# Kernel tuning notes

Measured on AMD Instinct MI355X. Metric: run time of the kernel, lower is better.

## Reference

```python
import jax, jax.numpy as jnp
import numpy as np

N, E, D, H = 50000, 800000, 128, 4
DH = D // H
BN_EPS = 1e-5


def setup_inputs() -> dict:
    key = jax.random.key(0)
    ks = jax.random.split(key, 16)
    s = 0.02
    inp = {
        "x": jax.random.normal(ks[0], (N, D), dtype=jnp.float32),
        "edge_index": jax.random.randint(ks[1], (2, E), 0, N, dtype=jnp.int64),
        "Wk": jax.random.normal(ks[2], (D, D), dtype=jnp.float32) * s,
        "bk": jnp.zeros((D,), jnp.float32),
        "Wm": jax.random.normal(ks[3], (D, D), dtype=jnp.float32) * s,
        "bm": jnp.zeros((D,), jnp.float32),
        "Wq": jax.random.normal(ks[4], (D, D), dtype=jnp.float32) * s,
        "bq": jnp.zeros((D,), jnp.float32),
        "W1": jax.random.normal(ks[5], (D, D), dtype=jnp.float32) * s,
        "b1": jnp.zeros((D,), jnp.float32),
        "gamma": jnp.ones((D,), jnp.float32),
        "beta": jnp.zeros((D,), jnp.float32),
        "W2": jax.random.normal(ks[6], (D, D), dtype=jnp.float32) * s,
        "b2": jnp.zeros((D,), jnp.float32),
    }
    return inp


def reference(x, edge_index, Wk, bk, Wm, bm, Wq, bq, W1, b1, gamma, beta, W2, b2):
    src = edge_index[0]  # [E] softmax segment key
    dst = edge_index[1]  # [E] aggregation target
    x_i = x[dst]         # [E, D] (torch code: X[1])
    x_j = x[src]         # [E, D] (torch code: X[0])

    key = (x_i @ Wk + bk).reshape(-1, H, DH)
    msg = (x_j @ Wm + bm).reshape(-1, H, DH)
    query = (x_j @ Wq + bq).reshape(-1, H, DH) / jnp.sqrt(jnp.float32(DH))

    scores = jnp.sum(query * key, axis=2)  # [E, H]

    # segment softmax over src node index (numerically stable)
    smax = jax.ops.segment_max(scores, src, num_segments=N)
    e = jnp.exp(scores - smax[src])
    ssum = jax.ops.segment_sum(e, src, num_segments=N)
    alpha = e / ssum[src]  # [E, H]

    # rescale by per-src-node edge count
    cnt = jax.ops.segment_sum(jnp.ones((scores.shape[0],), jnp.float32), src, num_segments=N)
    alpha = alpha * cnt[src][:, None]

    out_e = (msg * alpha[:, :, None]).reshape(-1, D)  # [E, D]
    out = jax.ops.segment_sum(out_e, dst, num_segments=N)  # [N, D]

    # MLP: Linear -> BatchNorm1d (training-mode batch stats) -> ReLU -> Linear
    h = out @ W1 + b1
    mean = jnp.mean(h, axis=0)
    var = jnp.var(h, axis=0)  # biased variance, as torch BN uses for normalization
    h = (h - mean) * jax.lax.rsqrt(var + BN_EPS) * gamma + beta
    h = jax.nn.relu(h)
    return h @ W2 + b2
```

## Files before the change

### kernel.cpp

```cpp
#include <hip/hip_runtime.h>
#include <hip/hip_bf16.h>

#define N_NODES 50000
#define N_EDGES 800000
#define DIM 128
#define NHEAD 4
#define GEMM_BLOCKS 782
#define RANK_ILP 8
#define RANK_BLOCKS 391

typedef __bf16 bf16x8 __attribute__((ext_vector_type(8)));
typedef __bf16 bf16x2 __attribute__((ext_vector_type(2)));
typedef float f32x4 __attribute__((ext_vector_type(4)));

struct WPtrs { const float* w[5]; };

__global__ __launch_bounds__(256) void prep_weights(WPtrs P, __bf16* __restrict__ Wt)
{
  __shared__ __bf16 tileT[16][136];
  const int mat = blockIdx.x >> 3, sl = blockIdx.x & 7;
  const float* W = P.w[mat];
  const int col0 = sl * 16;
  const int t = threadIdx.x;
  #pragma unroll
  for (int i = 0; i < 8; ++i) {
    int id = t + i * 256;
    int k = id >> 4, c = id & 15;
    tileT[c][k] = (__bf16)W[k * 128 + col0 + c];
  }
  __syncthreads();
  int c = t >> 4, kb = t & 15;
  bf16x8 v = *(const bf16x8*)&tileT[c][kb * 8];
  *(bf16x8*)&Wt[(size_t)mat * 16384 + (size_t)(col0 + c) * 128 + kb * 8] = v;
}


__device__ __forceinline__ void stage_Wt_half(const __bf16* __restrict__ Wt,
    int half, __bf16 (*wLDS)[136])
{
  const int t = threadIdx.x;
  const __bf16* base = Wt + (size_t)half * 64 * 128;
  #pragma unroll
  for (int i = 0; i < 4; ++i) {
    int id = t + i * 256;
    int col = id >> 4, kb = id & 15;
    bf16x8 v = ((const bf16x8*)(base + (size_t)col * 128))[kb];
    *(bf16x8*)&wLDS[col][kb * 8] = v;
  }
}

__device__ __forceinline__ void stage_A_f32(const float* __restrict__ A, int row0,
    int nrows, __bf16 (*aLDS)[136])
{
  const int t = threadIdx.x;
  #pragma unroll
  for (int i = 0; i < 4; ++i) {
    int id = t + i * 256;
    int r = id >> 4, cb = id & 15;
    int gr = row0 + r;
    float4 v0 = make_float4(0.f, 0.f, 0.f, 0.f), v1 = v0;
    if (gr < nrows) {
      const float4* row = (const float4*)(A + (size_t)gr * DIM);
      v0 = row[cb * 2];
      v1 = row[cb * 2 + 1];
    }
    bf16x8 o;
    o[0] = (__bf16)v0.x; o[1] = (__bf16)v0.y; o[2] = (__bf16)v0.z; o[3] = (__bf16)v0.w;
    o[4] = (__bf16)v1.x; o[5] = (__bf16)v1.y; o[6] = (__bf16)v1.z; o[7] = (__bf16)v1.w;
    *(bf16x8*)&aLDS[r][cb * 8] = o;
  }
}

__device__ __forceinline__ void mfma_half(const __bf16 (*aLDS)[136],
    const __bf16 (*wLDS)[136], int half, f32x4 acc[8])
{
  const int lane = threadIdx.x & 63, wave = threadIdx.x >> 6;
  const int m = lane & 15, q = lane >> 4;
  #pragma unroll
  for (int kt = 0; kt < 4; ++kt) {
    bf16x8 a = *(const bf16x8*)&aLDS[wave * 16 + m][kt * 32 + q * 8];
    #pragma unroll
    for (int ct = 0; ct < 4; ++ct) {
      bf16x8 b = *(const bf16x8*)&wLDS[ct * 16 + m][kt * 32 + q * 8];
      acc[half * 4 + ct] =
          __builtin_amdgcn_mfma_f32_16x16x32_bf16(a, b, acc[half * 4 + ct], 0, 0, 0);
    }
  }
}

template <typename OutT>
__device__ __forceinline__ void store_tile(f32x4 acc[8],
    const float* __restrict__ bias, float scale, OutT* __restrict__ C,
    int row0, int nrows)
{
  const int lane = threadIdx.x & 63, wave = threadIdx.x >> 6;
  const int m = lane & 15, q = lane >> 4;
  #pragma unroll
  for (int j = 0; j < 8; ++j) {
    int col = (j >> 2) * 64 + (j & 3) * 16 + m;
    float bv = bias[col];
    #pragma unroll
    for (int r = 0; r < 4; ++r) {
      int row = row0 + wave * 16 + q * 4 + r;
      if (row < nrows) C[(size_t)row * DIM + col] = (OutT)((acc[j][r] + bv) * scale);
    }
  }
}

__device__ __forceinline__ void gemm_pass(const __bf16 (*aLDS)[136],
    __bf16 (*wLDS)[136], const __bf16* __restrict__ Wt, f32x4 acc[8])
{
  #pragma unroll
  for (int i = 0; i < 8; ++i) acc[i] = (f32x4){0.f, 0.f, 0.f, 0.f};
  stage_Wt_half(Wt, 0, wLDS);
  __syncthreads();
  mfma_half(aLDS, wLDS, 0, acc);
  __syncthreads();
  stage_Wt_half(Wt, 1, wLDS);
  __syncthreads();
  mfma_half(aLDS, wLDS, 1, acc);
}

__global__ __launch_bounds__(256) void qkm_gemm(const float* __restrict__ A,
    const __bf16* __restrict__ Wt,
    const float* __restrict__ bk, const float* __restrict__ bm,
    const float* __restrict__ bq,
    __bf16* __restrict__ Kn, __bf16* __restrict__ Mn, __bf16* __restrict__ Qn)
{
  __shared__ __bf16 aLDS[64][136];
  __shared__ __bf16 wLDS[64][136];
  const int row0 = blockIdx.x * 64;
  f32x4 acc[8];

  stage_A_f32(A, row0, N_NODES, aLDS);
  gemm_pass(aLDS, wLDS, Wt, acc);
  store_tile<__bf16>(acc, bk, 1.0f, Kn, row0, N_NODES);
  __syncthreads();
  gemm_pass(aLDS, wLDS, Wt + 16384, acc);
  store_tile<__bf16>(acc, bm, 1.0f, Mn, row0, N_NODES);
  __syncthreads();
  gemm_pass(aLDS, wLDS, Wt + 32768, acc);
  store_tile<__bf16>(acc, bq, 0.17677669529663689f, Qn, row0, N_NODES);
}

__global__ __launch_bounds__(256) void edge_rank(const int* __restrict__ ei,
    int* __restrict__ deg, int2* __restrict__ rank)
{
  const int base = blockIdx.x * (256 * RANK_ILP) + threadIdx.x;
  int s[RANK_ILP], d[RANK_ILP], rS[RANK_ILP], rD[RANK_ILP];
  #pragma unroll
  for (int i = 0; i < RANK_ILP; ++i) {
    int e = base + i * 256;
    if (e < N_EDGES) { s[i] = ei[e]; d[i] = ei[N_EDGES + e]; }
  }
  #pragma unroll
  for (int i = 0; i < RANK_ILP; ++i) {
    int e = base + i * 256;
    if (e < N_EDGES) rS[i] = atomicAdd(&deg[s[i]], 1);
  }
  #pragma unroll
  for (int i = 0; i < RANK_ILP; ++i) {
    int e = base + i * 256;
    if (e < N_EDGES) rD[i] = atomicAdd(&deg[N_NODES + d[i]], 1);
  }
  #pragma unroll
  for (int i = 0; i < RANK_ILP; ++i) {
    int e = base + i * 256;
    if (e < N_EDGES) rank[e] = make_int2(rS[i], rD[i]);
  }
}

__global__ __launch_bounds__(256) void scan_pass1(const int* __restrict__ deg,
    int* __restrict__ bsum, int total)
{
  int i = blockIdx.x * 256 + threadIdx.x;
  int v = (i < total) ? deg[i] : 0;
  __shared__ int s[256];
  s[threadIdx.x] = v; __syncthreads();
  for (int o = 128; o > 0; o >>= 1) {
    if (threadIdx.x < o) s[threadIdx.x] += s[threadIdx.x + o];
    __syncthreads();
  }
  if (threadIdx.x == 0) bsum[blockIdx.x] = s[0];
}

__global__ __launch_bounds__(512) void scan_pass2(int* __restrict__ bsum, int nblocks)
{
  int t = threadIdx.x;
  __shared__ int s[512];
  int v = (t < nblocks) ? bsum[t] : 0;
  s[t] = v; __syncthreads();
  for (int o = 1; o < 512; o <<= 1) {
    int x = (t >= o) ? s[t - o] : 0;
    __syncthreads();
    s[t] += x;
    __syncthreads();
  }
  bsum[t] = s[t] - v;
}

__global__ __launch_bounds__(256) void scan_pass3(const int* __restrict__ deg,
    const int* __restrict__ bsum, int* __restrict__ starts, int total)
{
  int t = threadIdx.x, i = blockIdx.x * 256 + t;
  int v = (i < total) ? deg[i] : 0;
  __shared__ int s[256];
  s[t] = v; __syncthreads();
  for (int o = 1; o < 256; o <<= 1) {
    int x = (t >= o) ? s[t - o] : 0;
    __syncthreads();
    s[t] += x;
    __syncthreads();
  }
  if (i < total) starts[i] = bsum[blockIdx.x] + s[t] - v;
}

__global__ __launch_bounds__(256) void edge_place(const int* __restrict__ ei,
    const int2* __restrict__ rank, const int* __restrict__ starts,
    int* __restrict__ elistS, int2* __restrict__ elistD)
{
  int e = blockIdx.x * 256 + threadIdx.x;
  int src = ei[e], dst = ei[N_EDGES + e];
  int2 r = rank[e];
  int pS = starts[src] + r.x;
  int pD = starts[N_NODES + dst] - N_EDGES + r.y;
  elistS[pS] = dst;
  elistD[pD] = make_int2(src, pS);
}

__global__ __launch_bounds__(256) void src_scores(const int* __restrict__ starts,
    const int* __restrict__ degS, const int* __restrict__ elistS,
    const __bf16* __restrict__ Qn, const __bf16* __restrict__ Kn,
    __bf16* __restrict__ Mn, float* __restrict__ wexp)
{
  const int wave = threadIdx.x >> 6, l = threadIdx.x & 63;
  const int n = blockIdx.x * 4 + wave;
  const int g = l >> 4, il = l & 15;
  const int h = il >> 2;
  const int beg = starts[n], end = beg + degS[n];
  if (beg == end) return;

  bf16x8 q8 = ((const bf16x8*)(Qn + (size_t)n * DIM))[il];
  float wsum = 0.f;

  for (int p0 = beg; p0 < end; p0 += 16) {
    int pp[4], dd[4];
    #pragma unroll
    for (int u = 0; u < 4; ++u) {
      pp[u] = p0 + u * 4 + g;
      dd[u] = elistS[min(pp[u], end - 1)];
    }
    bf16x8 kk[4];
    #pragma unroll
    for (int u = 0; u < 4; ++u)
      kk[u] = ((const bf16x8*)(Kn + (size_t)dd[u] * DIM))[il];
    #pragma unroll
    for (int u = 0; u < 4; ++u) {
      float pr = 0.f;
      #pragma unroll
      for (int j = 0; j < 8; ++j) pr += (float)q8[j] * (float)kk[u][j];
      pr += __shfl_xor(pr, 1);
      pr += __shfl_xor(pr, 2);
      float w = (pp[u] < end) ? __expf(pr) : 0.f;
      wsum += w;
      if ((pp[u] < end) && (il & 3) == 0) wexp[(size_t)pp[u] * NHEAD + h] = w;
    }
  }
  wsum += __shfl_xor(wsum, 16);
  wsum += __shfl_xor(wsum, 32);
  float factor = (float)(end - beg) / wsum;

  float fm = __shfl(factor, (l >> 4) << 2);
  bf16x2* mrow = (bf16x2*)(Mn + (size_t)n * DIM);
  bf16x2 mv = mrow[l];
  mv[0] = (__bf16)((float)mv[0] * fm);
  mv[1] = (__bf16)((float)mv[1] * fm);
  mrow[l] = mv;
}

__global__ __launch_bounds__(256) void dst_aggregate(const int* __restrict__ startsD,
    const int* __restrict__ degD, const int2* __restrict__ elistD,
    const __bf16* __restrict__ Mn, const float* __restrict__ wexp,
    float* __restrict__ agg)
{
  const int wave = threadIdx.x >> 6, l = threadIdx.x & 63;
  const int n = blockIdx.x * 4 + wave;
  const int g = l >> 4, il = l & 15;
  const int h = il >> 2;
  const int beg = startsD[n] - N_EDGES, end = beg + degD[n];

  float acc[8];
  #pragma unroll
  for (int j = 0; j < 8; ++j) acc[j] = 0.f;

  for (int q0 = beg; q0 < end; q0 += 16) {
    int qq[4]; int2 ss[4];
    #pragma unroll
    for (int u = 0; u < 4; ++u) {
      qq[u] = q0 + u * 4 + g;
      ss[u] = elistD[min(qq[u], end - 1)];
    }
    float aa[4];
    #pragma unroll
    for (int u = 0; u < 4; ++u) aa[u] = wexp[(size_t)ss[u].y * NHEAD + h];
    bf16x8 mm[4];
    #pragma unroll
    for (int u = 0; u < 4; ++u)
      mm[u] = ((const bf16x8*)(Mn + (size_t)ss[u].x * DIM))[il];
    #pragma unroll
    for (int u = 0; u < 4; ++u) {
      float av = (qq[u] < end) ? aa[u] : 0.f;
      #pragma unroll
      for (int j = 0; j < 8; ++j) acc[j] += (float)mm[u][j] * av;
    }
  }
  #pragma unroll
  for (int j = 0; j < 8; ++j) {
    acc[j] += __shfl_xor(acc[j], 16);
    acc[j] += __shfl_xor(acc[j], 32);
  }
  if (g == 0) {
    float* row = agg + (size_t)n * DIM + il * 8;
    *(float4*)row       = make_float4(acc[0], acc[1], acc[2], acc[3]);
    *(float4*)(row + 4) = make_float4(acc[4], acc[5], acc[6], acc[7]);
  }
}

__global__ __launch_bounds__(256) void gemm_stats(const float* __restrict__ A,
    const __bf16* __restrict__ Wt, const float* __restrict__ bias,
    __bf16* __restrict__ C, float* __restrict__ colsum, float* __restrict__ colsq)
{
  __shared__ __bf16 aLDS[64][136];
  __shared__ __bf16 wLDS[64][136];
  __shared__ float csum[128], csq[128];
  const int t = threadIdx.x;
  const int row0 = blockIdx.x * 64;

  stage_A_f32(A, row0, N_NODES, aLDS);
  if (t < 128) { csum[t] = 0.f; csq[t] = 0.f; }
  f32x4 acc[8];
  gemm_pass(aLDS, wLDS, Wt, acc);

  const int lane = t & 63, wave = t >> 6;
  const int m = lane & 15, q = lane >> 4;
  #pragma unroll
  for (int j = 0; j < 8; ++j) {
    int col = (j >> 2) * 64 + (j & 3) * 16 + m;
    float bv = bias[col];
    float s = 0.f, s2 = 0.f;
    #pragma unroll
    for (int r = 0; r < 4; ++r) {
      int row = row0 + wave * 16 + q * 4 + r;
      float hv = acc[j][r] + bv;
      if (row < N_NODES) {
        C[(size_t)row * DIM + col] = (__bf16)hv;
        s += hv; s2 += hv * hv;
      }
    }
    s  += __shfl_xor(s, 16);  s  += __shfl_xor(s, 32);
    s2 += __shfl_xor(s2, 16); s2 += __shfl_xor(s2, 32);
    if (q == 0) {
      atomicAdd(&csum[col], s);
      atomicAdd(&csq[col], s2);
    }
  }
  __syncthreads();
  if (t < 128) {
    atomicAdd(&colsum[t], csum[t]);
    atomicAdd(&colsq[t], csq[t]);
  }
}

__global__ __launch_bounds__(256) void gemm_bn(const __bf16* __restrict__ A,
    const __bf16* __restrict__ Wt, const float* __restrict__ bias,
    float* __restrict__ C, const float* __restrict__ colsum,
    const float* __restrict__ colsq, const float* __restrict__ gamma,
    const float* __restrict__ beta)
{
  __shared__ __bf16 aLDS[64][136];
  __shared__ __bf16 wLDS[64][136];
  __shared__ float sA[128], sB[128];
  const int t = threadIdx.x;
  const int row0 = blockIdx.x * 64;

  if (t < 128) {
    float mean = colsum[t] * (1.0f / N_NODES);
    float var = colsq[t] * (1.0f / N_NODES) - mean * mean;
    float inv = rsqrtf(var + 1e-5f);
    float a = gamma[t] * inv;
    sA[t] = a;
    sB[t] = beta[t] - mean * a;
  }
  __syncthreads();

  {
    const int cb = t & 15;
    float sa[8], sb[8];
    #pragma unroll
    for (int j = 0; j < 8; ++j) { sa[j] = sA[cb * 8 + j]; sb[j] = sB[cb * 8 + j]; }
    #pragma unroll
    for (int i = 0; i < 4; ++i) {
      int id = t + i * 256;
      int r = id >> 4;
      int gr = row0 + r;
      bf16x8 v = {};
      if (gr < N_NODES) v = ((const bf16x8*)(A + (size_t)gr * DIM))[cb];
      bf16x8 o;
      #pragma unroll
      for (int j = 0; j < 8; ++j)
        o[j] = (__bf16)fmaxf((float)v[j] * sa[j] + sb[j], 0.f);
      *(bf16x8*)&aLDS[r][cb * 8] = o;
    }
  }
  f32x4 acc[8];
  gemm_pass(aLDS, wLDS, Wt, acc);
  store_tile<float>(acc, bias, 1.0f, C, row0, N_NODES);
}

extern "C" void kernel_launch(void* const* d_in, const int* in_sizes, int n_in,
                              void* d_out, int out_size, void* d_ws, size_t ws_size,
                              hipStream_t stream) {
  const float* x     = (const float*)d_in[0];
  const int*   ei    = (const int*)d_in[1];
  const float* Wk    = (const float*)d_in[2];
  const float* bk    = (const float*)d_in[3];
  const float* Wm    = (const float*)d_in[4];
  const float* bm    = (const float*)d_in[5];
  const float* Wq    = (const float*)d_in[6];
  const float* bq    = (const float*)d_in[7];
  const float* W1    = (const float*)d_in[8];
  const float* b1    = (const float*)d_in[9];
  const float* gamma = (const float*)d_in[10];
  const float* beta  = (const float*)d_in[11];
  const float* W2    = (const float*)d_in[12];
  const float* b2    = (const float*)d_in[13];

  float* ws = (float*)d_ws;
  const size_t ND  = (size_t)N_NODES * DIM;
  const size_t NDh = ND / 2;
  const size_t EH  = (size_t)N_EDGES * NHEAD;
  const int    N2  = 2 * N_NODES;

  __bf16* Kn   = (__bf16*)ws;
  __bf16* Mn   = (__bf16*)(ws + NDh);
  __bf16* Qn   = (__bf16*)(ws + 2 * NDh);
  float*  agg  = ws + 3 * NDh;
  __bf16* h1   = (__bf16*)(agg + ND);
  float*  wexp = (float*)(h1 + ND);
  int2*   rank   = (int2*)(wexp + EH);
  int2*   elistD = rank + N_EDGES;
  int*    elistS = (int*)(elistD + N_EDGES);
  int*    deg    = elistS + N_EDGES;
  float*  colsum = (float*)(deg + N2);
  float*  colsq  = colsum + 128;
  int*    starts = (int*)(colsq + 128);
  int*    bsum   = starts + N2;
  __bf16* Wt     = (__bf16*)(bsum + 512);
  float*  outp   = (float*)d_out;

  hipMemsetAsync(deg, 0, (N2 + 256) * sizeof(int), stream);

  const int scan_blocks = (N2 + 255) / 256;
  const int edge_blocks = N_EDGES / 256;
  const int node_blocks = N_NODES / 4;

  WPtrs wp; wp.w[0] = Wk; wp.w[1] = Wm; wp.w[2] = Wq; wp.w[3] = W1; wp.w[4] = W2;
  prep_weights<<<40, 256, 0, stream>>>(wp, Wt);

  edge_rank<<<RANK_BLOCKS, 256, 0, stream>>>(ei, deg, rank);
  scan_pass1<<<scan_blocks, 256, 0, stream>>>(deg, bsum, N2);
  scan_pass2<<<1, 512, 0, stream>>>(bsum, scan_blocks);
  scan_pass3<<<scan_blocks, 256, 0, stream>>>(deg, bsum, starts, N2);
  edge_place<<<edge_blocks, 256, 0, stream>>>(ei, rank, starts, elistS, elistD);

  qkm_gemm<<<GEMM_BLOCKS, 256, 0, stream>>>(x, Wt, bk, bm, bq, Kn, Mn, Qn);

  src_scores<<<node_blocks, 256, 0, stream>>>(starts, deg, elistS, Qn, Kn, Mn, wexp);
  dst_aggregate<<<node_blocks, 256, 0, stream>>>(starts + N_NODES, deg + N_NODES,
                                                 elistD, Mn, wexp, agg);

  gemm_stats<<<GEMM_BLOCKS, 256, 0, stream>>>(agg, Wt + 3 * 16384, b1, h1,
                                              colsum, colsq);
  gemm_bn<<<GEMM_BLOCKS, 256, 0, stream>>>(h1, Wt + 4 * 16384, b2, outp,
                                           colsum, colsq, gamma, beta);
}
```

Baseline: 350.1 us.

## Merge edge ranking with QKM GEMM in one launch and store aggregate as bf16

Puts the atomic edge-ranking blocks and the Q/K/M projection GEMM blocks into a single heterogeneous kernel, so the latency-bound atomic work and the compute-bound GEMM can run on the GPU at the same time instead of one after the other. Separately, the aggregated node features are now stored as bf16 instead of fp32, which halves the write in dst_aggregate and the read in gemm_stats (that GEMM already rounds its input to bf16). The cost is extra rounding of the aggregate before it is staged, which matches the rounding that was already applied in LDS, and a larger grid whose GEMM blocks use more LDS than the ranking blocks need.

```diff
diff --git a/kernel.cpp b/kernel.cpp
--- a/kernel.cpp
+++ b/kernel.cpp
@@ -71,6 +71,21 @@
   }
 }
 
+__device__ __forceinline__ void stage_A_bf16(const __bf16* __restrict__ A, int row0,
+    int nrows, __bf16 (*aLDS)[136])
+{
+  const int t = threadIdx.x;
+  #pragma unroll
+  for (int i = 0; i < 4; ++i) {
+    int id = t + i * 256;
+    int r = id >> 4, cb = id & 15;
+    int gr = row0 + r;
+    bf16x8 v = {};
+    if (gr < nrows) v = ((const bf16x8*)(A + (size_t)gr * DIM))[cb];
+    *(bf16x8*)&aLDS[r][cb * 8] = v;
+  }
+}
+
 __device__ __forceinline__ void mfma_half(const __bf16 (*aLDS)[136],
     const __bf16 (*wLDS)[136], int half, f32x4 acc[8])
 {
@@ -121,52 +136,52 @@
   mfma_half(aLDS, wLDS, 1, acc);
 }
 
-__global__ __launch_bounds__(256) void qkm_gemm(const float* __restrict__ A,
-    const __bf16* __restrict__ Wt,
+__global__ __launch_bounds__(256) void fat1(const int* __restrict__ ei,
+    int* __restrict__ deg, int2* __restrict__ rank,
+    const __bf16* __restrict__ Wt, const float* __restrict__ x,
     const float* __restrict__ bk, const float* __restrict__ bm,
     const float* __restrict__ bq,
     __bf16* __restrict__ Kn, __bf16* __restrict__ Mn, __bf16* __restrict__ Qn)
 {
   __shared__ __bf16 aLDS[64][136];
   __shared__ __bf16 wLDS[64][136];
-  const int row0 = blockIdx.x * 64;
-  f32x4 acc[8];
-
-  stage_A_f32(A, row0, N_NODES, aLDS);
-  gemm_pass(aLDS, wLDS, Wt, acc);
-  store_tile<__bf16>(acc, bk, 1.0f, Kn, row0, N_NODES);
-  __syncthreads();
-  gemm_pass(aLDS, wLDS, Wt + 16384, acc);
-  store_tile<__bf16>(acc, bm, 1.0f, Mn, row0, N_NODES);
-  __syncthreads();
-  gemm_pass(aLDS, wLDS, Wt + 32768, acc);
-  store_tile<__bf16>(acc, bq, 0.17677669529663689f, Qn, row0, N_NODES);
-}
-
-__global__ __launch_bounds__(256) void edge_rank(const int* __restrict__ ei,
-    int* __restrict__ deg, int2* __restrict__ rank)
-{
-  const int base = blockIdx.x * (256 * RANK_ILP) + threadIdx.x;
-  int s[RANK_ILP], d[RANK_ILP], rS[RANK_ILP], rD[RANK_ILP];
-  #pragma unroll
-  for (int i = 0; i < RANK_ILP; ++i) {
-    int e = base + i * 256;
-    if (e < N_EDGES) { s[i] = ei[e]; d[i] = ei[N_EDGES + e]; }
-  }
-  #pragma unroll
-  for (int i = 0; i < RANK_ILP; ++i) {
-    int e = base + i * 256;
-    if (e < N_EDGES) rS[i] = atomicAdd(&deg[s[i]], 1);
-  }
-  #pragma unroll
-  for (int i = 0; i < RANK_ILP; ++i) {
-    int e = base + i * 256;
-    if (e < N_EDGES) rD[i] = atomicAdd(&deg[N_NODES + d[i]], 1);
-  }
-  #pragma unroll
-  for (int i = 0; i < RANK_ILP; ++i) {
-    int e = base + i * 256;
-    if (e < N_EDGES) rank[e] = make_int2(rS[i], rD[i]);
+  const int b = blockIdx.x, t = threadIdx.x;
+
+  if (b < RANK_BLOCKS) {
+    const int base = b * (256 * RANK_ILP) + t;
+    int s[RANK_ILP], d[RANK_ILP], rS[RANK_ILP], rD[RANK_ILP];
+    #pragma unroll
+    for (int i = 0; i < RANK_ILP; ++i) {
+      int e = base + i * 256;
+      if (e < N_EDGES) { s[i] = ei[e]; d[i] = ei[N_EDGES + e]; }
+    }
+    #pragma unroll
+    for (int i = 0; i < RANK_ILP; ++i) {
+      int e = base + i * 256;
+      if (e < N_EDGES) rS[i] = atomicAdd(&deg[s[i]], 1);
+    }
+    #pragma unroll
+    for (int i = 0; i < RANK_ILP; ++i) {
+      int e = base + i * 256;
+      if (e < N_EDGES) rD[i] = atomicAdd(&deg[N_NODES + d[i]], 1);
+    }
+    #pragma unroll
+    for (int i = 0; i < RANK_ILP; ++i) {
+      int e = base + i * 256;
+      if (e < N_EDGES) rank[e] = make_int2(rS[i], rD[i]);
+    }
+  } else {
+    const int row0 = (b - RANK_BLOCKS) * 64;
+    f32x4 acc[8];
+    stage_A_f32(x, row0, N_NODES, aLDS);
+    gemm_pass(aLDS, wLDS, Wt, acc);
+    store_tile<__bf16>(acc, bk, 1.0f, Kn, row0, N_NODES);
+    __syncthreads();
+    gemm_pass(aLDS, wLDS, Wt + 16384, acc);
+    store_tile<__bf16>(acc, bm, 1.0f, Mn, row0, N_NODES);
+    __syncthreads();
+    gemm_pass(aLDS, wLDS, Wt + 32768, acc);
+    store_tile<__bf16>(acc, bq, 0.17677669529663689f, Qn, row0, N_NODES);
   }
 }
 
@@ -281,7 +296,7 @@
 __global__ __launch_bounds__(256) void dst_aggregate(const int* __restrict__ startsD,
     const int* __restrict__ degD, const int2* __restrict__ elistD,
     const __bf16* __restrict__ Mn, const float* __restrict__ wexp,
-    float* __restrict__ agg)
+    __bf16* __restrict__ agg)
 {
   const int wave = threadIdx.x >> 6, l = threadIdx.x & 63;
   const int n = blockIdx.x * 4 + wave;
@@ -320,13 +335,14 @@
     acc[j] += __shfl_xor(acc[j], 32);
   }
   if (g == 0) {
-    float* row = agg + (size_t)n * DIM + il * 8;
-    *(float4*)row       = make_float4(acc[0], acc[1], acc[2], acc[3]);
-    *(float4*)(row + 4) = make_float4(acc[4], acc[5], acc[6], acc[7]);
-  }
-}
-
-__global__ __launch_bounds__(256) void gemm_stats(const float* __restrict__ A,
+    bf16x8 o;
+    #pragma unroll
+    for (int j = 0; j < 8; ++j) o[j] = (__bf16)acc[j];
+    *(bf16x8*)(agg + (size_t)n * DIM + il * 8) = o;
+  }
+}
+
+__global__ __launch_bounds__(256) void gemm_stats(const __bf16* __restrict__ A,
     const __bf16* __restrict__ Wt, const float* __restrict__ bias,
     __bf16* __restrict__ C, float* __restrict__ colsum, float* __restrict__ colsq)
 {
@@ -336,7 +352,7 @@
   const int t = threadIdx.x;
   const int row0 = blockIdx.x * 64;
 
-  stage_A_f32(A, row0, N_NODES, aLDS);
+  stage_A_bf16(A, row0, N_NODES, aLDS);
   if (t < 128) { csum[t] = 0.f; csq[t] = 0.f; }
   f32x4 acc[8];
   gemm_pass(aLDS, wLDS, Wt, acc);
@@ -444,9 +460,9 @@
   __bf16* Kn   = (__bf16*)ws;
   __bf16* Mn   = (__bf16*)(ws + NDh);
   __bf16* Qn   = (__bf16*)(ws + 2 * NDh);
-  float*  agg  = ws + 3 * NDh;
-  __bf16* h1   = (__bf16*)(agg + ND);
-  float*  wexp = (float*)(h1 + ND);
+  __bf16* agg  = (__bf16*)(ws + 3 * NDh);
+  __bf16* h1   = (__bf16*)(ws + 4 * NDh);
+  float*  wexp = ws + 5 * NDh;
   int2*   rank   = (int2*)(wexp + EH);
   int2*   elistD = rank + N_EDGES;
   int*    elistS = (int*)(elistD + N_EDGES);
@@ -467,14 +483,14 @@
   WPtrs wp; wp.w[0] = Wk; wp.w[1] = Wm; wp.w[2] = Wq; wp.w[3] = W1; wp.w[4] = W2;
   prep_weights<<<40, 256, 0, stream>>>(wp, Wt);
 
-  edge_rank<<<RANK_BLOCKS, 256, 0, stream>>>(ei, deg, rank);
+  fat1<<<RANK_BLOCKS + GEMM_BLOCKS, 256, 0, stream>>>(
+      ei, deg, rank, Wt, x, bk, bm, bq, Kn, Mn, Qn);
+
   scan_pass1<<<scan_blocks, 256, 0, stream>>>(deg, bsum, N2);
   scan_pass2<<<1, 512, 0, stream>>>(bsum, scan_blocks);
   scan_pass3<<<scan_blocks, 256, 0, stream>>>(deg, bsum, starts, N2);
   edge_place<<<edge_blocks, 256, 0, stream>>>(ei, rank, starts, elistS, elistD);
 
-  qkm_gemm<<<GEMM_BLOCKS, 256, 0, stream>>>(x, Wt, bk, bm, bq, Kn, Mn, Qn);
-
   src_scores<<<node_blocks, 256, 0, stream>>>(starts, deg, elistS, Qn, Kn, Mn, wexp);
   dst_aggregate<<<node_blocks, 256, 0, stream>>>(starts + N_NODES, deg + N_NODES,
                                                  elistD, Mn, wexp, agg);
```

Measured after the change: 336.3 us. -3.9%, faster.
